# Performance work log

Measured on AMD Instinct MI355X. Metric: run time of the kernel, lower is better.

## Reference

```python
import jax, jax.numpy as jnp
import numpy as np

FP8_MAX = 448.0  # max finite value of float8_e4m3fn


def quantize_tensorwise(x):
    """Tensorwise fp8 quantization: returns fp8 tensor and inverse scale."""
    amax = jnp.max(jnp.abs(x))
    inv_scale = jnp.maximum(amax, jnp.asarray(1e-12, x.dtype)) / FP8_MAX
    q = (x / inv_scale).astype(jnp.float8_e4m3fn)
    return q, inv_scale


def setup_inputs() -> dict:
    key = jax.random.key(0)
    k1, k2, k3 = jax.random.split(key, 3)
    x = jax.random.normal(k1, (4, 1024, 4096), dtype=jnp.float32)
    weight = jax.random.normal(k2, (4096, 4096), dtype=jnp.float32) * 0.02
    bias = jax.random.normal(k3, (4096,), dtype=jnp.float32)
    return {"x": x, "weight": weight, "bias": bias}


def reference(x, weight, bias):
    out_shape = (*x.shape[:-1], weight.shape[0])
    xm = x.reshape(-1, x.shape[-1])                    # [M, K]
    fp8_x, x_inv_scale = quantize_tensorwise(xm)       # fp8 input + tensorwise scale
    fp8_wt, w_inv_scale = quantize_tensorwise(weight.T)  # weight.t() quantized, [K, N]
    # fp8 GEMM with inline dequant: (fp8_x @ fp8_w.T) * sx * sw + bias
    acc = jnp.matmul(fp8_x.astype(jnp.float32), fp8_wt.astype(jnp.float32))
    out = acc * (x_inv_scale * w_inv_scale) + bias.astype(jnp.float32)
    return out.reshape(out_shape).astype(x.dtype)
```

## Files before the change

### kernel.cpp

```cpp
#include <hip/hip_runtime.h>
#include <hip/hip_bf16.h>
#include <stdint.h>

static constexpr int M = 4096, N = 4096, K = 4096;
static constexpr float FP8_MAX = 448.0f;

using f32x16 = __attribute__((ext_vector_type(16))) float;
using i32x4  = __attribute__((ext_vector_type(4))) int;
using i32x8  = __attribute__((ext_vector_type(8))) int;

static constexpr size_t AQ_OFF   = 0;
static constexpr size_t BQ_OFF   = (size_t)M * K;
static constexpr size_t AMAX_OFF = BQ_OFF + (size_t)N * K;

__global__ void init_amax_kernel(float* amax) {
    amax[0] = 0.0f;
    amax[1] = 0.0f;
}

__global__ __launch_bounds__(256) void amax_kernel(const float* __restrict__ x,
                                                   const float* __restrict__ w,
                                                   float* __restrict__ amax,
                                                   int n4_per_tensor,
                                                   int blocks_per_tensor) {
    const int tensor = blockIdx.x / blocks_per_tensor;
    const int blk    = blockIdx.x % blocks_per_tensor;
    const float4* src = (const float4*)(tensor == 0 ? x : w);

    float m = 0.0f;
    for (int i = blk * blockDim.x + threadIdx.x; i < n4_per_tensor;
         i += blocks_per_tensor * blockDim.x) {
        float4 v = src[i];
        m = fmaxf(m, fmaxf(fmaxf(fabsf(v.x), fabsf(v.y)),
                           fmaxf(fabsf(v.z), fabsf(v.w))));
    }
    #pragma unroll
    for (int off = 32; off >= 1; off >>= 1)
        m = fmaxf(m, __shfl_xor(m, off, 64));

    __shared__ float sm[4];
    const int lane = threadIdx.x & 63, wid = threadIdx.x >> 6;
    if (lane == 0) sm[wid] = m;
    __syncthreads();
    if (threadIdx.x == 0) {
        m = fmaxf(fmaxf(sm[0], sm[1]), fmaxf(sm[2], sm[3]));
        atomicMax((unsigned int*)&amax[tensor], __float_as_uint(m));
    }
}

__global__ __launch_bounds__(256) void quant_kernel(const float* __restrict__ x,
                                                    const float* __restrict__ w,
                                                    unsigned char* __restrict__ aq,
                                                    unsigned char* __restrict__ bq,
                                                    const float* __restrict__ amax,
                                                    int n4_per_tensor) {
    int gid = blockIdx.x * blockDim.x + threadIdx.x;
    const int tensor = (gid >= n4_per_tensor) ? 1 : 0;
    const int i = tensor ? gid - n4_per_tensor : gid;

    const float inv = fmaxf(amax[tensor], 1e-12f) / FP8_MAX;
    const float4* src = (const float4*)(tensor == 0 ? x : w);
    int* dst = (int*)(tensor == 0 ? aq : bq);

    float4 v = src[i];
    float q0 = v.x / inv, q1 = v.y / inv, q2 = v.z / inv, q3 = v.w / inv;
    int packed = __builtin_amdgcn_cvt_pk_fp8_f32(q0, q1, 0, false);
    packed     = __builtin_amdgcn_cvt_pk_fp8_f32(q2, q3, packed, true);
    dst[i] = packed;
}

static constexpr int BM = 256, BN = 256, BK = 64, DEPTH = 4, NT = K / BK;

__device__ __forceinline__ void gld_lds16(const void* g, void* l) {
    __builtin_amdgcn_global_load_lds(
        (const __attribute__((address_space(1))) void*)g,
        (__attribute__((address_space(3))) void*)l, 16, 0, 0);
}

struct BReg { i32x4 lo0, hi0, lo1, hi1; };

__global__ __launch_bounds__(512, 2) void gemm_kernel(const unsigned char* __restrict__ Aq,
                                                      const unsigned char* __restrict__ Bq,
                                                      const float* __restrict__ amax,
                                                      const float* __restrict__ bias,
                                                      float* __restrict__ out) {
    __shared__ unsigned char lds[DEPTH][BM * BK];

    const int tid  = threadIdx.x;
    const int lane = tid & 63;
    const int w    = tid >> 6;
    const int wr   = w >> 2, wc = w & 3;

    const int bid = blockIdx.x;
    const int swz = (bid & 7) * 32 + (bid >> 3);
    const int brow = (swz >> 4) * BM;
    const int bcol = (swz & 15) * BN;

    const float sx = fmaxf(amax[0], 1e-12f) / FP8_MAX;
    const float sw = fmaxf(amax[1], 1e-12f) / FP8_MAX;
    const float scale = sx * sw;

    const int r4    = lane >> 2;
    const int row0  = w * 16 + r4;
    const int chk   = ((lane & 3) ^ ((row0 >> 1) & 3)) * 16;
    const unsigned char* Abase = Aq + (size_t)brow * K;

    const int frow = lane & 31;
    const int swzr = (frow >> 1) & 3;
    const int c0   = (lane >> 5) * 2;
    const int off0 = ((c0 ^ swzr) << 4);
    const int off1 = (((c0 + 1) ^ swzr) << 4);

    const unsigned char* Bp0 = Bq + (size_t)(bcol + wc * 64 + frow) * K      + (lane >> 5) * 32;
    const unsigned char* Bp1 = Bq + (size_t)(bcol + wc * 64 + 32 + frow) * K + (lane >> 5) * 32;

    f32x16 acc[4][2] = {};

#define STAGE_A(t, d)                                                                          \
    do {                                                                                       \
        const size_t _k0 = (size_t)(t) * BK;                                                   \
        gld_lds16(Abase + (size_t)row0 * K + _k0 + chk,         &lds[d][w * 1024]);            \
        gld_lds16(Abase + (size_t)(row0 + 128) * K + _k0 + chk, &lds[d][8192 + w * 1024]);     \
    } while (0)

#define GLOAD_B(t, BR)                                                         \
    do {                                                                       \
        const size_t _kb = (size_t)(t) * BK;                                   \
        BR.lo0 = *(const i32x4*)(Bp0 + _kb);                                   \
        BR.hi0 = *(const i32x4*)(Bp0 + _kb + 16);                              \
        BR.lo1 = *(const i32x4*)(Bp1 + _kb);                                   \
        BR.hi1 = *(const i32x4*)(Bp1 + _kb + 16);                              \
    } while (0)

#define ITER(t, rs, ss, BRcur, BRld)                                           \
    do {                                                                       \
        asm volatile("s_waitcnt vmcnt(6)" ::: "memory");                       \
        __builtin_amdgcn_s_barrier();                                          \
        STAGE_A(((t) + 3 < NT) ? (t) + 3 : NT - 1, ss);                        \
        GLOAD_B(((t) + 2 < NT) ? (t) + 2 : NT - 1, BRld);                      \
        i32x8 _aF[4];                                                          \
        _Pragma("unroll")                                                      \
        for (int _mt = 0; _mt < 4; ++_mt) {                                    \
            const unsigned char* _p = &lds[rs][(wr * 128 + _mt * 32 + frow) * BK]; \
            i32x4 _lo = *(const i32x4*)(_p + off0);                            \
            i32x4 _hi = *(const i32x4*)(_p + off1);                            \
            _aF[_mt] = __builtin_shufflevector(_lo, _hi, 0, 1, 2, 3, 4, 5, 6, 7); \
        }                                                                      \
        i32x8 _b0 = __builtin_shufflevector(BRcur.lo0, BRcur.hi0, 0, 1, 2, 3, 4, 5, 6, 7); \
        i32x8 _b1 = __builtin_shufflevector(BRcur.lo1, BRcur.hi1, 0, 1, 2, 3, 4, 5, 6, 7); \
        __builtin_amdgcn_s_setprio(1);                                         \
        _Pragma("unroll")                                                      \
        for (int _mt = 0; _mt < 4; ++_mt) {                                    \
            acc[_mt][0] = __builtin_amdgcn_mfma_scale_f32_32x32x64_f8f6f4(     \
                _aF[_mt], _b0, acc[_mt][0], 0, 0, 0, 0x7F, 0, 0x7F);           \
            acc[_mt][1] = __builtin_amdgcn_mfma_scale_f32_32x32x64_f8f6f4(     \
                _aF[_mt], _b1, acc[_mt][1], 0, 0, 0, 0x7F, 0, 0x7F);           \
        }                                                                      \
        __builtin_amdgcn_s_setprio(0);                                         \
        asm volatile("s_waitcnt lgkmcnt(0)" ::: "memory");                     \
        __builtin_amdgcn_sched_barrier(0);                                     \
    } while (0)

    BReg br0, br1, br2, br3;

    STAGE_A(0, 0);
    GLOAD_B(0, br0);
    STAGE_A(1, 1);
    GLOAD_B(1, br1);
    STAGE_A(2, 2);

    for (int t = 0; t < NT; t += 4) {
        ITER(t + 0, 0, 3, br0, br2);
        ITER(t + 1, 1, 0, br1, br3);
        ITER(t + 2, 2, 1, br2, br0);
        ITER(t + 3, 3, 2, br3, br1);
    }
#undef ITER
#undef GLOAD_B
#undef STAGE_A

    #pragma unroll
    for (int mt = 0; mt < 4; ++mt) {
        const int rbase = brow + wr * 128 + mt * 32 + 4 * (lane >> 5);
        #pragma unroll
        for (int nt2 = 0; nt2 < 2; ++nt2) {
            const int col = bcol + wc * 64 + nt2 * 32 + (lane & 31);
            const float b = bias[col];
            #pragma unroll
            for (int reg = 0; reg < 16; ++reg) {
                const int row = rbase + (reg & 3) + 8 * (reg >> 2);
                out[(size_t)row * N + col] = acc[mt][nt2][reg] * scale + b;
            }
        }
    }
}

extern "C" void kernel_launch(void* const* d_in, const int* in_sizes, int n_in,
                              void* d_out, int out_size, void* d_ws, size_t ws_size,
                              hipStream_t stream) {
    const float* x    = (const float*)d_in[0];
    const float* w    = (const float*)d_in[1];
    const float* bias = (const float*)d_in[2];
    float* out = (float*)d_out;

    unsigned char* aq = (unsigned char*)d_ws + AQ_OFF;
    unsigned char* bq = (unsigned char*)d_ws + BQ_OFF;
    float* amax = (float*)((unsigned char*)d_ws + AMAX_OFF);

    const int n4 = (M * K) / 4;

    init_amax_kernel<<<1, 1, 0, stream>>>(amax);

    const int blocks_per_tensor = 512;
    amax_kernel<<<2 * blocks_per_tensor, 256, 0, stream>>>(x, w, amax, n4, blocks_per_tensor);

    const int quant_blocks = (2 * n4) / 256;
    quant_kernel<<<quant_blocks, 256, 0, stream>>>(x, w, aq, bq, amax, n4);

    gemm_kernel<<<256, 512, 0, stream>>>(aq, bq, amax, bias, out);
}
```

Baseline: 162.5 us.

## Pre-swizzle quantized weight into MFMA fragment layout for coalesced B loads

The quant kernel now writes the fp8 weight in a blocked layout where each 32-row by 64-k tile is stored as contiguous per-lane 32-byte fragments. The GEMM's B register loads then read fully contiguous 2 KB chunks instead of strided rows. The wait count and scheduling barriers are adjusted to match, and the init kernel is replaced with hipMemsetAsync. The cost is a scattered-store write pattern in the quant kernel, plus a changed vmcnt threshold that could affect correctness or overlap.

```diff
diff --git a/kernel.cpp b/kernel.cpp
--- a/kernel.cpp
+++ b/kernel.cpp
@@ -12,11 +12,6 @@
 static constexpr size_t AQ_OFF   = 0;
 static constexpr size_t BQ_OFF   = (size_t)M * K;
 static constexpr size_t AMAX_OFF = BQ_OFF + (size_t)N * K;
-
-__global__ void init_amax_kernel(float* amax) {
-    amax[0] = 0.0f;
-    amax[1] = 0.0f;
-}
 
 __global__ __launch_bounds__(256) void amax_kernel(const float* __restrict__ x,
                                                    const float* __restrict__ w,
@@ -60,13 +55,21 @@
 
     const float inv = fmaxf(amax[tensor], 1e-12f) / FP8_MAX;
     const float4* src = (const float4*)(tensor == 0 ? x : w);
-    int* dst = (int*)(tensor == 0 ? aq : bq);
 
     float4 v = src[i];
     float q0 = v.x / inv, q1 = v.y / inv, q2 = v.z / inv, q3 = v.w / inv;
     int packed = __builtin_amdgcn_cvt_pk_fp8_f32(q0, q1, 0, false);
     packed     = __builtin_amdgcn_cvt_pk_fp8_f32(q2, q3, packed, true);
-    dst[i] = packed;
+
+    if (tensor == 0) {
+        ((int*)aq)[i] = packed;
+    } else {
+        const int n  = i >> 10;
+        const int k0 = (i & 1023) * 4;
+        const int blk = (n >> 5) * (K / 64) + (k0 >> 6);
+        const int ln  = (n & 31) + 32 * ((k0 >> 5) & 1);
+        ((int*)bq)[blk * 512 + ln * 8 + ((k0 >> 2) & 7)] = packed;
+    }
 }
 
 static constexpr int BM = 256, BN = 256, BK = 64, DEPTH = 4, NT = K / BK;
@@ -111,8 +114,10 @@
     const int off0 = ((c0 ^ swzr) << 4);
     const int off1 = (((c0 + 1) ^ swzr) << 4);
 
-    const unsigned char* Bp0 = Bq + (size_t)(bcol + wc * 64 + frow) * K      + (lane >> 5) * 32;
-    const unsigned char* Bp1 = Bq + (size_t)(bcol + wc * 64 + 32 + frow) * K + (lane >> 5) * 32;
+    const unsigned char* Bf0 =
+        Bq + (size_t)((bcol >> 5) + wc * 2 + 0) * (K / 64) * 2048 + (size_t)lane * 32;
+    const unsigned char* Bf1 =
+        Bq + (size_t)((bcol >> 5) + wc * 2 + 1) * (K / 64) * 2048 + (size_t)lane * 32;
 
     f32x16 acc[4][2] = {};
 
@@ -125,17 +130,18 @@
 
 #define GLOAD_B(t, BR)                                                         \
     do {                                                                       \
-        const size_t _kb = (size_t)(t) * BK;                                   \
-        BR.lo0 = *(const i32x4*)(Bp0 + _kb);                                   \
-        BR.hi0 = *(const i32x4*)(Bp0 + _kb + 16);                              \
-        BR.lo1 = *(const i32x4*)(Bp1 + _kb);                                   \
-        BR.hi1 = *(const i32x4*)(Bp1 + _kb + 16);                              \
+        const size_t _o = (size_t)(t) * 2048;                                  \
+        BR.lo0 = *(const i32x4*)(Bf0 + _o);                                    \
+        BR.hi0 = *(const i32x4*)(Bf0 + _o + 16);                               \
+        BR.lo1 = *(const i32x4*)(Bf1 + _o);                                    \
+        BR.hi1 = *(const i32x4*)(Bf1 + _o + 16);                               \
     } while (0)
 
 #define ITER(t, rs, ss, BRcur, BRld)                                           \
     do {                                                                       \
-        asm volatile("s_waitcnt vmcnt(6)" ::: "memory");                       \
+        asm volatile("s_waitcnt vmcnt(12)" ::: "memory");                      \
         __builtin_amdgcn_s_barrier();                                          \
+        __builtin_amdgcn_sched_barrier(0);                                     \
         STAGE_A(((t) + 3 < NT) ? (t) + 3 : NT - 1, ss);                        \
         GLOAD_B(((t) + 2 < NT) ? (t) + 2 : NT - 1, BRld);                      \
         i32x8 _aF[4];                                                          \
@@ -168,6 +174,9 @@
     STAGE_A(1, 1);
     GLOAD_B(1, br1);
     STAGE_A(2, 2);
+    asm volatile("s_waitcnt vmcnt(0)" ::: "memory");
+    __builtin_amdgcn_s_barrier();
+    __builtin_amdgcn_sched_barrier(0);
 
     for (int t = 0; t < NT; t += 4) {
         ITER(t + 0, 0, 3, br0, br2);
@@ -209,7 +218,7 @@
 
     const int n4 = (M * K) / 4;
 
-    init_amax_kernel<<<1, 1, 0, stream>>>(amax);
+    hipMemsetAsync(amax, 0, 2 * sizeof(float), stream);
 
     const int blocks_per_tensor = 512;
     amax_kernel<<<2 * blocks_per_tensor, 256, 0, stream>>>(x, w, amax, n4, blocks_per_tensor);
```

After: 138.2 us. 14.9% less time.
